# Kernel optimization log

Hardware: AMD Instinct MI355X
Metric: run time of the kernel (lower is better)

## Reference

```python
import jax, jax.numpy as jnp
import numpy as np

B, N, D, H = 4, 2048, 512, 8
DH = D // H
DFF = 4 * D
EPS = 1e-5


def layernorm(x, g, b):
    mu = jnp.mean(x, axis=-1, keepdims=True)
    var = jnp.mean((x - mu) ** 2, axis=-1, keepdims=True)
    return (x - mu) * jax.lax.rsqrt(var + EPS) * g + b


def setup_inputs() -> dict:
    key = jax.random.key(0)
    ks = jax.random.split(key, 8)
    s = 0.02
    return {
        "x": jax.random.normal(ks[0], (B, N, D), dtype=jnp.float32),
        "ln1_g": jnp.ones((D,), jnp.float32),
        "ln1_b": jnp.zeros((D,), jnp.float32),
        "Wqkv": jax.random.normal(ks[1], (D, 3 * D), jnp.float32) * s,
        "bqkv": jnp.zeros((3 * D,), jnp.float32),
        "Wproj": jax.random.normal(ks[2], (D, D), jnp.float32) * s,
        "bproj": jnp.zeros((D,), jnp.float32),
        "ln2_g": jnp.ones((D,), jnp.float32),
        "ln2_b": jnp.zeros((D,), jnp.float32),
        "W1": jax.random.normal(ks[3], (D, DFF), jnp.float32) * s,
        "b1": jnp.zeros((DFF,), jnp.float32),
        "W2": jax.random.normal(ks[4], (DFF, D), jnp.float32) * s,
        "b2": jnp.zeros((D,), jnp.float32),
    }


def reference(x, ln1_g, ln1_b, Wqkv, bqkv, Wproj, bproj, ln2_g, ln2_b, W1, b1, W2, b2):
    scale = DH ** -0.5
    # --- PreNorm + MHSA + residual ---
    h = layernorm(x, ln1_g, ln1_b)                      # [B,N,D]
    qkv = h @ Wqkv + bqkv                               # [B,N,3D]
    qkv = qkv.reshape(B, N, 3, H, DH)
    q, k, v = qkv[:, :, 0], qkv[:, :, 1], qkv[:, :, 2]  # [B,N,H,DH]
    attn = jnp.einsum("bnhd,bmhd->bhnm", q, k) * scale  # [B,H,N,N]
    attn = jax.nn.softmax(attn, axis=-1)
    out = jnp.einsum("bhnm,bmhd->bnhd", attn, v).reshape(B, N, D)
    x = x + out @ Wproj + bproj
    # --- PreNorm + GELU-MLP + residual ---
    h2 = layernorm(x, ln2_g, ln2_b)
    ff = jax.nn.gelu(h2 @ W1 + b1, approximate=False) @ W2 + b2
    return x + ff
```

## Files before the change

kernel.cpp:

```cpp
#include <hip/hip_runtime.h>

#define B_ 4
#define N_ 2048
#define D_ 512
#define H_ 8
#define DH_ 64
#define ROWS_ 8192
#define KSCALE 0.18033688011112042f

typedef float f32x4 __attribute__((ext_vector_type(4)));
typedef short short8v __attribute__((ext_vector_type(8)));
typedef short short4v __attribute__((ext_vector_type(4)));
typedef unsigned uint4v __attribute__((ext_vector_type(4)));

__device__ __forceinline__ short f2bf(float f) {
    unsigned u = __builtin_bit_cast(unsigned, f);
    u += 0x7FFFu + ((u >> 16) & 1u);
    return (short)(u >> 16);
}

__device__ __forceinline__ unsigned cvtpk_bf16(float lo, float hi) {
    unsigned r;
    asm("v_cvt_pk_bf16_f32 %0, %1, %2" : "=v"(r) : "v"(lo), "v"(hi));
    return r;
}

__device__ __forceinline__ void gload16(const void* g, void* l) {
    __builtin_amdgcn_global_load_lds(
        (const __attribute__((address_space(1))) unsigned int*)g,
        (__attribute__((address_space(3))) unsigned int*)l, 16, 0, 0);
}

__device__ __forceinline__ void waitvm0_barrier() {
    asm volatile("s_waitcnt vmcnt(0)" ::: "memory");
    __builtin_amdgcn_s_barrier();
}

__global__ __launch_bounds__(256) void ln_bf16_kernel(const float* __restrict__ x,
                                                      const float* __restrict__ g,
                                                      const float* __restrict__ bb,
                                                      short* __restrict__ out) {
    int wave = threadIdx.x >> 6;
    int lane = threadIdx.x & 63;
    int row  = blockIdx.x * 4 + wave;
    const float* xr = x + (size_t)row * D_;

    float4 v0 = ((const float4*)xr)[lane * 2 + 0];
    float4 v1 = ((const float4*)xr)[lane * 2 + 1];

    float s = v0.x + v0.y + v0.z + v0.w + v1.x + v1.y + v1.z + v1.w;
    #pragma unroll
    for (int off = 32; off; off >>= 1) s += __shfl_xor(s, off, 64);
    float mu = s * (1.0f / D_);

    float d0 = v0.x - mu, d1 = v0.y - mu, d2 = v0.z - mu, d3 = v0.w - mu;
    float d4 = v1.x - mu, d5 = v1.y - mu, d6 = v1.z - mu, d7 = v1.w - mu;
    float vs = d0*d0 + d1*d1 + d2*d2 + d3*d3 + d4*d4 + d5*d5 + d6*d6 + d7*d7;
    #pragma unroll
    for (int off = 32; off; off >>= 1) vs += __shfl_xor(vs, off, 64);
    float rstd = rsqrtf(vs * (1.0f / D_) + 1e-5f);

    float4 g0 = ((const float4*)g)[lane * 2 + 0];
    float4 g1 = ((const float4*)g)[lane * 2 + 1];
    float4 b0 = ((const float4*)bb)[lane * 2 + 0];
    float4 b1 = ((const float4*)bb)[lane * 2 + 1];

    short8v ov;
    ov[0] = f2bf(d0 * rstd * g0.x + b0.x);
    ov[1] = f2bf(d1 * rstd * g0.y + b0.y);
    ov[2] = f2bf(d2 * rstd * g0.z + b0.z);
    ov[3] = f2bf(d3 * rstd * g0.w + b0.w);
    ov[4] = f2bf(d4 * rstd * g1.x + b1.x);
    ov[5] = f2bf(d5 * rstd * g1.y + b1.y);
    ov[6] = f2bf(d6 * rstd * g1.z + b1.z);
    ov[7] = f2bf(d7 * rstd * g1.w + b1.w);
    *(short8v*)&out[(size_t)row * D_ + lane * 8] = ov;
}

__global__ __launch_bounds__(256) void wt_kernel(const float* __restrict__ W,
                                                 short* __restrict__ WT,
                                                 int K, int N) {
    __shared__ short Ts[64][72];
    int tid = threadIdx.x;
    int n0 = blockIdx.x * 64, k0 = blockIdx.y * 64;

    #pragma unroll
    for (int i = 0; i < 4; ++i) {
        int idx = tid + i * 256;
        int k = idx >> 4, nq = (idx & 15) * 4;
        float4 wv = *(const float4*)&W[(size_t)(k0 + k) * N + n0 + nq];
        short4v t;
        t[0] = f2bf(wv.x); t[1] = f2bf(wv.y); t[2] = f2bf(wv.z); t[3] = f2bf(wv.w);
        *(short4v*)&Ts[k][nq] = t;
    }
    __syncthreads();

    int n = tid >> 2, kq = (tid & 3) * 16;
    short8v o0, o1;
    #pragma unroll
    for (int j = 0; j < 8; ++j) { o0[j] = Ts[kq + j][n]; o1[j] = Ts[kq + 8 + j][n]; }
    *(short8v*)&WT[(size_t)(n0 + n) * K + k0 + kq]     = o0;
    *(short8v*)&WT[(size_t)(n0 + n) * K + k0 + kq + 8] = o1;
}

template<bool GELU, bool RESID, bool OUTBF, bool QKVMODE>
__global__ __launch_bounds__(256) void gemm_bf16(const short* __restrict__ A,
                                                 const short* __restrict__ BT,
                                                 const float* __restrict__ bias,
                                                 const float* __restrict__ resid,
                                                 float* __restrict__ Cf,
                                                 short* __restrict__ Cb,
                                                 short* __restrict__ vtg,
                                                 int M, int N, int K) {
    __shared__ short As[2][8192];
    __shared__ short Bs[2][4096];
    int tid = threadIdx.x;
    int l = tid & 63, w = tid >> 6;
    int wr = w >> 1, wc = w & 1;
    int l15 = l & 15, lg = l >> 4;
    int row0 = blockIdx.x * 128, col0 = blockIdx.y * 64;

    int rsub = l >> 3;
    int kq_  = ((l & 7) ^ rsub) * 8;
    int rsw  = l15 & 7;

    const short* ap[4];
    const short* bp[2];
    #pragma unroll
    for (int i = 0; i < 4; ++i)
        ap[i] = A + (size_t)(row0 + i * 32 + w * 8 + rsub) * K + kq_;
    bp[0] = BT + (size_t)(col0 + w * 8 + rsub) * K + kq_;
    bp[1] = BT + (size_t)(col0 + 32 + w * 8 + rsub) * K + kq_;

    int aoff0 = (wr * 64 + l15) * 64 + ((lg ^ rsw)) * 8;
    int aoff1 = (wr * 64 + l15) * 64 + (((4 + lg) ^ rsw)) * 8;
    int boff0 = (wc * 32 + l15) * 64 + ((lg ^ rsw)) * 8;
    int boff1 = (wc * 32 + l15) * 64 + (((4 + lg) ^ rsw)) * 8;

    const f32x4 zero4 = {0.f, 0.f, 0.f, 0.f};
    f32x4 acc[4][2];
    #pragma unroll
    for (int m = 0; m < 4; ++m)
        #pragma unroll
        for (int n = 0; n < 2; ++n) acc[m][n] = zero4;

    auto stage = [&](int bf) {
        #pragma unroll
        for (int i = 0; i < 4; ++i) {
            gload16(ap[i], &As[bf][(i * 4 + w) * 512]);
            ap[i] += 64;
        }
        gload16(bp[0], &Bs[bf][w * 512]);       bp[0] += 64;
        gload16(bp[1], &Bs[bf][(4 + w) * 512]); bp[1] += 64;
    };

    auto compute = [&](int bf) {
        #pragma unroll
        for (int ks = 0; ks < 2; ++ks) {
            short8v a[4], bfr[2];
            #pragma unroll
            for (int m = 0; m < 4; ++m)
                a[m] = *(const short8v*)&As[bf][(ks ? aoff1 : aoff0) + m * 1024];
            #pragma unroll
            for (int n = 0; n < 2; ++n)
                bfr[n] = *(const short8v*)&Bs[bf][(ks ? boff1 : boff0) + n * 1024];
            __builtin_amdgcn_s_setprio(1);
            #pragma unroll
            for (int m = 0; m < 4; ++m)
                #pragma unroll
                for (int n = 0; n < 2; ++n)
                    acc[m][n] = __builtin_amdgcn_mfma_f32_16x16x32_bf16(a[m], bfr[n], acc[m][n], 0, 0, 0);
            __builtin_amdgcn_s_setprio(0);
        }
    };

    stage(0);
    waitvm0_barrier();

    int NH = K >> 7;
    for (int t2 = 0; t2 < NH; ++t2) {
        stage(1);
        compute(0);
        waitvm0_barrier();
        if (t2 + 1 < NH) stage(0);
        compute(1);
        waitvm0_barrier();
    }

    if (QKVMODE && col0 >= 1024) {
        int b = row0 >> 11;
        int nb = row0 & 2047;
        #pragma unroll
        for (int n = 0; n < 2; ++n) {
            int col = col0 + wc * 32 + n * 16 + l15;
            float bv = bias[col];
            int hd = col - 1024;
            size_t vrow = (size_t)(b * 512 + hd) * N_;
            #pragma unroll
            for (int m = 0; m < 4; ++m) {
                int nbase = nb + wr * 64 + m * 16 + lg * 4;
                uint2 uu;
                uu.x = cvtpk_bf16(acc[m][n][0] + bv, acc[m][n][1] + bv);
                uu.y = cvtpk_bf16(acc[m][n][2] + bv, acc[m][n][3] + bv);
                *(uint2*)&vtg[vrow + nbase] = uu;
            }
        }
        return;
    }

    float qscl = (QKVMODE && col0 < 512) ? KSCALE : 1.0f;
    #pragma unroll
    for (int n = 0; n < 2; ++n) {
        int col = col0 + wc * 32 + n * 16 + l15;
        float bv = bias[col];
        #pragma unroll
        for (int m = 0; m < 4; ++m) {
            #pragma unroll
            for (int i = 0; i < 4; ++i) {
                int row = row0 + wr * 64 + m * 16 + lg * 4 + i;
                size_t off = (size_t)row * N + col;
                float v = acc[m][n][i] + bv;
                if (RESID) v += resid[off];
                if (GELU)  v = 0.5f * v * (1.0f + erff(v * 0.70710678118654752f));
                if (QKVMODE) v *= qscl;
                if (OUTBF) Cb[off] = f2bf(v);
                else       Cf[off] = v;
            }
        }
    }
}

__global__ __launch_bounds__(256) void fattn_bf16(const short* __restrict__ qkvb,
                                                  const short* __restrict__ vtg,
                                                  short* __restrict__ attnout) {
    __shared__ short Ks[2][4096];
    __shared__ short Vt[2][4096];

    int tid = threadIdx.x;
    int l = tid & 63, w = tid >> 6;
    int l15 = l & 15, lg = l >> 4;
    int bh = blockIdx.x, qt = blockIdx.y;
    int b = bh >> 3, h = bh & 7;
    int n0 = qt * 64;
    int qb = w * 16;

    int hK = ((l15 >> 2) << 1) | (l15 & 1);
    int hV = l15 & 7;
    int kperm = ((l15 >> 2) << 3) + (l15 & 3);

    int koff0 = kperm * 64 + (lg ^ hK) * 8;
    int koff1 = kperm * 64 + (((4 + lg) ^ hK)) * 8;
    int voff0 = l15 * 64 + (lg ^ hV) * 8;
    int voff1 = l15 * 64 + (((4 + lg) ^ hV)) * 8;

    short8v bQ[2];
    #pragma unroll
    for (int ks = 0; ks < 2; ++ks)
        bQ[ks] = *(const short8v*)
            &qkvb[(size_t)(b * N_ + n0 + qb + l15) * 1536 + h * 64 + ks * 32 + lg * 8];

    short8v ones;
    #pragma unroll
    for (int j = 0; j < 8; ++j) ones[j] = (short)0x3F80;

    const f32x4 zero4 = {0.f, 0.f, 0.f, 0.f};
    f32x4 o[4], l_acc = zero4;
    #pragma unroll
    for (int df = 0; df < 4; ++df) o[df] = zero4;

    int lr = l >> 3, lc = l & 7;
    const short* kp[2];
    const short* vp[2];
    #pragma unroll
    for (int i = 0; i < 2; ++i) {
        int g = w * 2 + i, r = g * 8 + lr;
        int hKs = ((g & 3) << 1) | (lr & 1);
        kp[i] = &qkvb[(size_t)(b * N_ + r) * 1536 + 512 + h * 64 + ((lc ^ hKs) << 3)];
        vp[i] = &vtg[((size_t)bh * 64 + r) * N_ + ((lc ^ lr) << 3)];
    }

    auto stage = [&](int bf) {
        #pragma unroll
        for (int i = 0; i < 2; ++i) {
            int g = w * 2 + i;
            gload16(kp[i], &Ks[bf][g * 512]); kp[i] += 64 * 1536;
            gload16(vp[i], &Vt[bf][g * 512]); vp[i] += 64;
        }
    };

    auto compute = [&](int bf) {
        f32x4 s[4];
        #pragma unroll
        for (int kf = 0; kf < 4; ++kf) {
            short8v aK0 = *(const short8v*)&Ks[bf][koff0 + (kf >> 1) * 2048 + (kf & 1) * 256];
            short8v aK1 = *(const short8v*)&Ks[bf][koff1 + (kf >> 1) * 2048 + (kf & 1) * 256];
            __builtin_amdgcn_s_setprio(1);
            s[kf] = __builtin_amdgcn_mfma_f32_16x16x32_bf16(aK0, bQ[0], zero4, 0, 0, 0);
            s[kf] = __builtin_amdgcn_mfma_f32_16x16x32_bf16(aK1, bQ[1], s[kf], 0, 0, 0);
            __builtin_amdgcn_s_setprio(0);
        }

        short8v bP[2];
        #pragma unroll
        for (int kf = 0; kf < 4; ++kf)
            #pragma unroll
            for (int i = 0; i < 4; ++i)
                s[kf][i] = exp2f(s[kf][i]);
        #pragma unroll
        for (int ks = 0; ks < 2; ++ks) {
            uint4v u;
            u[0] = cvtpk_bf16(s[2 * ks][0],     s[2 * ks][1]);
            u[1] = cvtpk_bf16(s[2 * ks][2],     s[2 * ks][3]);
            u[2] = cvtpk_bf16(s[2 * ks + 1][0], s[2 * ks + 1][1]);
            u[3] = cvtpk_bf16(s[2 * ks + 1][2], s[2 * ks + 1][3]);
            bP[ks] = __builtin_bit_cast(short8v, u);
        }

        __builtin_amdgcn_s_setprio(1);
        l_acc = __builtin_amdgcn_mfma_f32_16x16x32_bf16(ones, bP[0], l_acc, 0, 0, 0);
        l_acc = __builtin_amdgcn_mfma_f32_16x16x32_bf16(ones, bP[1], l_acc, 0, 0, 0);
        __builtin_amdgcn_s_setprio(0);
        #pragma unroll
        for (int df = 0; df < 4; ++df) {
            short8v aV0 = *(const short8v*)&Vt[bf][voff0 + df * 1024];
            short8v aV1 = *(const short8v*)&Vt[bf][voff1 + df * 1024];
            __builtin_amdgcn_s_setprio(1);
            o[df] = __builtin_amdgcn_mfma_f32_16x16x32_bf16(aV0, bP[0], o[df], 0, 0, 0);
            o[df] = __builtin_amdgcn_mfma_f32_16x16x32_bf16(aV1, bP[1], o[df], 0, 0, 0);
            __builtin_amdgcn_s_setprio(0);
        }
    };

    stage(0);
    waitvm0_barrier();

    for (int t2 = 0; t2 < 16; ++t2) {
        stage(1);
        compute(0);
        waitvm0_barrier();
        if (t2 + 1 < 16) stage(0);
        compute(1);
        waitvm0_barrier();
    }

    {
        float linv = 1.0f / l_acc[0];
        size_t rowb = (size_t)(b * N_ + n0 + qb + l15) * D_ + h * 64;
        #pragma unroll
        for (int df = 0; df < 4; ++df) {
            uint2 uu;
            uu.x = cvtpk_bf16(o[df][0] * linv, o[df][1] * linv);
            uu.y = cvtpk_bf16(o[df][2] * linv, o[df][3] * linv);
            *(uint2*)&attnout[rowb + df * 16 + lg * 4] = uu;
        }
    }
}

extern "C" void kernel_launch(void* const* d_in, const int* in_sizes, int n_in,
                              void* d_out, int out_size, void* d_ws, size_t ws_size,
                              hipStream_t stream) {
    const float* x      = (const float*)d_in[0];
    const float* ln1_g  = (const float*)d_in[1];
    const float* ln1_b  = (const float*)d_in[2];
    const float* Wqkv   = (const float*)d_in[3];
    const float* bqkv   = (const float*)d_in[4];
    const float* Wproj  = (const float*)d_in[5];
    const float* bproj  = (const float*)d_in[6];
    const float* ln2_g  = (const float*)d_in[7];
    const float* ln2_b  = (const float*)d_in[8];
    const float* W1     = (const float*)d_in[9];
    const float* b1     = (const float*)d_in[10];
    const float* W2     = (const float*)d_in[11];
    const float* b2     = (const float*)d_in[12];
    float* out = (float*)d_out;

    char* ws = (char*)d_ws;
    short* h_bf    = (short*)(ws + (size_t)0);
    short* qkv_bf  = (short*)(ws + ((size_t)8  << 20));
    short* vtg     = (short*)(ws + ((size_t)32 << 20));
    short* attn_bf = (short*)(ws + ((size_t)40 << 20));
    float* x2      = (float*)(ws + ((size_t)48 << 20));
    short* h2_bf   = (short*)(ws + ((size_t)64 << 20));
    short* ffh_bf  = (short*)(ws + ((size_t)72 << 20));
    short* WTqkv   = (short*)(ws + ((size_t)104 << 20));
    short* WTproj  = (short*)(ws + ((size_t)106 << 20));
    short* WT1     = (short*)(ws + ((size_t)108 << 20));
    short* WT2     = (short*)(ws + ((size_t)110 << 20));

    dim3 blk(256);

    wt_kernel<<<dim3(24, 8),  blk, 0, stream>>>(Wqkv,  WTqkv,  512,  1536);
    wt_kernel<<<dim3(8, 8),   blk, 0, stream>>>(Wproj, WTproj, 512,  512);
    wt_kernel<<<dim3(32, 8),  blk, 0, stream>>>(W1,    WT1,    512,  2048);
    wt_kernel<<<dim3(8, 32),  blk, 0, stream>>>(W2,    WT2,    2048, 512);

    ln_bf16_kernel<<<ROWS_ / 4, blk, 0, stream>>>(x, ln1_g, ln1_b, h_bf);

    gemm_bf16<false, false, true, true><<<dim3(64, 24), blk, 0, stream>>>(
        h_bf, WTqkv, bqkv, nullptr, nullptr, qkv_bf, vtg, ROWS_, 1536, 512);

    fattn_bf16<<<dim3(32, 32), blk, 0, stream>>>(qkv_bf, vtg, attn_bf);

    gemm_bf16<false, true, false, false><<<dim3(64, 8), blk, 0, stream>>>(
        attn_bf, WTproj, bproj, x, x2, nullptr, nullptr, ROWS_, 512, 512);

    ln_bf16_kernel<<<ROWS_ / 4, blk, 0, stream>>>(x2, ln2_g, ln2_b, h2_bf);

    gemm_bf16<true, false, true, false><<<dim3(64, 32), blk, 0, stream>>>(
        h2_bf, WT1, b1, nullptr, nullptr, ffh_bf, nullptr, ROWS_, 2048, 512);

    gemm_bf16<false, true, false, false><<<dim3(64, 8), blk, 0, stream>>>(
        ffh_bf, WT2, b2, x2, out, nullptr, nullptr, ROWS_, 512, 2048);
}
```

Before: 183.2 us.

## Process two query sub-tiles per wave in flash attention to reuse K/V tiles

Each flash-attention block now covers 128 query rows instead of 64, with each wave holding two 16-row Q fragments and reusing every K and V LDS fragment for both. This halves the number of blocks and the K/V global-to-LDS traffic per query, and doubles the MFMA work per LDS read. In exchange it raises register pressure (double accumulators and score tiles) and gives 512 blocks instead of 1024, which may reduce occupancy and load balance on the GPU.

```diff
diff --git a/kernel.cpp b/kernel.cpp
--- a/kernel.cpp
+++ b/kernel.cpp
@@ -241,8 +241,8 @@
     int l15 = l & 15, lg = l >> 4;
     int bh = blockIdx.x, qt = blockIdx.y;
     int b = bh >> 3, h = bh & 7;
-    int n0 = qt * 64;
-    int qb = w * 16;
+    int n0 = qt * 128;
+    int qb = w * 32;
 
     int hK = ((l15 >> 2) << 1) | (l15 & 1);
     int hV = l15 & 7;
@@ -253,20 +253,26 @@
     int voff0 = l15 * 64 + (lg ^ hV) * 8;
     int voff1 = l15 * 64 + (((4 + lg) ^ hV)) * 8;
 
-    short8v bQ[2];
-    #pragma unroll
-    for (int ks = 0; ks < 2; ++ks)
-        bQ[ks] = *(const short8v*)
-            &qkvb[(size_t)(b * N_ + n0 + qb + l15) * 1536 + h * 64 + ks * 32 + lg * 8];
+    short8v bQ[2][2];
+    #pragma unroll
+    for (int qi = 0; qi < 2; ++qi)
+        #pragma unroll
+        for (int ks = 0; ks < 2; ++ks)
+            bQ[qi][ks] = *(const short8v*)
+                &qkvb[(size_t)(b * N_ + n0 + qb + qi * 16 + l15) * 1536 + h * 64 + ks * 32 + lg * 8];
 
     short8v ones;
     #pragma unroll
     for (int j = 0; j < 8; ++j) ones[j] = (short)0x3F80;
 
     const f32x4 zero4 = {0.f, 0.f, 0.f, 0.f};
-    f32x4 o[4], l_acc = zero4;
-    #pragma unroll
-    for (int df = 0; df < 4; ++df) o[df] = zero4;
+    f32x4 o[2][4], l_acc[2];
+    #pragma unroll
+    for (int qi = 0; qi < 2; ++qi) {
+        l_acc[qi] = zero4;
+        #pragma unroll
+        for (int df = 0; df < 4; ++df) o[qi][df] = zero4;
+    }
 
     int lr = l >> 3, lc = l & 7;
     const short* kp[2];
@@ -289,44 +295,56 @@
     };
 
     auto compute = [&](int bf) {
-        f32x4 s[4];
+        f32x4 s[2][4];
         #pragma unroll
         for (int kf = 0; kf < 4; ++kf) {
             short8v aK0 = *(const short8v*)&Ks[bf][koff0 + (kf >> 1) * 2048 + (kf & 1) * 256];
             short8v aK1 = *(const short8v*)&Ks[bf][koff1 + (kf >> 1) * 2048 + (kf & 1) * 256];
             __builtin_amdgcn_s_setprio(1);
-            s[kf] = __builtin_amdgcn_mfma_f32_16x16x32_bf16(aK0, bQ[0], zero4, 0, 0, 0);
-            s[kf] = __builtin_amdgcn_mfma_f32_16x16x32_bf16(aK1, bQ[1], s[kf], 0, 0, 0);
+            #pragma unroll
+            for (int qi = 0; qi < 2; ++qi) {
+                s[qi][kf] = __builtin_amdgcn_mfma_f32_16x16x32_bf16(aK0, bQ[qi][0], zero4, 0, 0, 0);
+                s[qi][kf] = __builtin_amdgcn_mfma_f32_16x16x32_bf16(aK1, bQ[qi][1], s[qi][kf], 0, 0, 0);
+            }
             __builtin_amdgcn_s_setprio(0);
         }
 
-        short8v bP[2];
-        #pragma unroll
-        for (int kf = 0; kf < 4; ++kf)
-            #pragma unroll
-            for (int i = 0; i < 4; ++i)
-                s[kf][i] = exp2f(s[kf][i]);
-        #pragma unroll
-        for (int ks = 0; ks < 2; ++ks) {
-            uint4v u;
-            u[0] = cvtpk_bf16(s[2 * ks][0],     s[2 * ks][1]);
-            u[1] = cvtpk_bf16(s[2 * ks][2],     s[2 * ks][3]);
-            u[2] = cvtpk_bf16(s[2 * ks + 1][0], s[2 * ks + 1][1]);
-            u[3] = cvtpk_bf16(s[2 * ks + 1][2], s[2 * ks + 1][3]);
-            bP[ks] = __builtin_bit_cast(short8v, u);
+        short8v bP[2][2];
+        #pragma unroll
+        for (int qi = 0; qi < 2; ++qi) {
+            #pragma unroll
+            for (int kf = 0; kf < 4; ++kf)
+                #pragma unroll
+                for (int i = 0; i < 4; ++i)
+                    s[qi][kf][i] = exp2f(s[qi][kf][i]);
+            #pragma unroll
+            for (int ks = 0; ks < 2; ++ks) {
+                uint4v u;
+                u[0] = cvtpk_bf16(s[qi][2 * ks][0],     s[qi][2 * ks][1]);
+                u[1] = cvtpk_bf16(s[qi][2 * ks][2],     s[qi][2 * ks][3]);
+                u[2] = cvtpk_bf16(s[qi][2 * ks + 1][0], s[qi][2 * ks + 1][1]);
+                u[3] = cvtpk_bf16(s[qi][2 * ks + 1][2], s[qi][2 * ks + 1][3]);
+                bP[qi][ks] = __builtin_bit_cast(short8v, u);
+            }
         }
 
         __builtin_amdgcn_s_setprio(1);
-        l_acc = __builtin_amdgcn_mfma_f32_16x16x32_bf16(ones, bP[0], l_acc, 0, 0, 0);
-        l_acc = __builtin_amdgcn_mfma_f32_16x16x32_bf16(ones, bP[1], l_acc, 0, 0, 0);
+        #pragma unroll
+        for (int qi = 0; qi < 2; ++qi) {
+            l_acc[qi] = __builtin_amdgcn_mfma_f32_16x16x32_bf16(ones, bP[qi][0], l_acc[qi], 0, 0, 0);
+            l_acc[qi] = __builtin_amdgcn_mfma_f32_16x16x32_bf16(ones, bP[qi][1], l_acc[qi], 0, 0, 0);
+        }
         __builtin_amdgcn_s_setprio(0);
         #pragma unroll
         for (int df = 0; df < 4; ++df) {
             short8v aV0 = *(const short8v*)&Vt[bf][voff0 + df * 1024];
             short8v aV1 = *(const short8v*)&Vt[bf][voff1 + df * 1024];
             __builtin_amdgcn_s_setprio(1);
-            o[df] = __builtin_amdgcn_mfma_f32_16x16x32_bf16(aV0, bP[0], o[df], 0, 0, 0);
-            o[df] = __builtin_amdgcn_mfma_f32_16x16x32_bf16(aV1, bP[1], o[df], 0, 0, 0);
+            #pragma unroll
+            for (int qi = 0; qi < 2; ++qi) {
+                o[qi][df] = __builtin_amdgcn_mfma_f32_16x16x32_bf16(aV0, bP[qi][0], o[qi][df], 0, 0, 0);
+                o[qi][df] = __builtin_amdgcn_mfma_f32_16x16x32_bf16(aV1, bP[qi][1], o[qi][df], 0, 0, 0);
+            }
             __builtin_amdgcn_s_setprio(0);
         }
     };
@@ -343,14 +361,15 @@
         waitvm0_barrier();
     }
 
-    {
-        float linv = 1.0f / l_acc[0];
-        size_t rowb = (size_t)(b * N_ + n0 + qb + l15) * D_ + h * 64;
+    #pragma unroll
+    for (int qi = 0; qi < 2; ++qi) {
+        float linv = 1.0f / l_acc[qi][0];
+        size_t rowb = (size_t)(b * N_ + n0 + qb + qi * 16 + l15) * D_ + h * 64;
         #pragma unroll
         for (int df = 0; df < 4; ++df) {
             uint2 uu;
-            uu.x = cvtpk_bf16(o[df][0] * linv, o[df][1] * linv);
-            uu.y = cvtpk_bf16(o[df][2] * linv, o[df][3] * linv);
+            uu.x = cvtpk_bf16(o[qi][df][0] * linv, o[qi][df][1] * linv);
+            uu.y = cvtpk_bf16(o[qi][df][2] * linv, o[qi][df][3] * linv);
             *(uint2*)&attnout[rowb + df * 16 + lg * 4] = uu;
         }
     }
@@ -399,7 +418,7 @@
     gemm_bf16<false, false, true, true><<<dim3(64, 24), blk, 0, stream>>>(
         h_bf, WTqkv, bqkv, nullptr, nullptr, qkv_bf, vtg, ROWS_, 1536, 512);
 
-    fattn_bf16<<<dim3(32, 32), blk, 0, stream>>>(qkv_bf, vtg, attn_bf);
+    fattn_bf16<<<dim3(32, 16), blk, 0, stream>>>(qkv_bf, vtg, attn_bf);
 
     gemm_bf16<false, true, false, false><<<dim3(64, 8), blk, 0, stream>>>(
         attn_bf, WTproj, bproj, x, x2, nullptr, nullptr, ROWS_, 512, 512);
```

Measured after the change: 177.7 us. -3.0%, faster.
